# Kernel optimization log

Measured on AMD Instinct MI355X. Metric: run time of the kernel, lower is better.

The kernel has to match this reference:

```python
import jax, jax.numpy as jnp
import numpy as np

D_MODEL = 1024
N_HEAD = 16
DIM_PER_HEAD = D_MODEL // N_HEAD
B, S = 8, 1024


def setup_inputs() -> dict:
    key = jax.random.key(0)
    ks = jax.random.split(key, 12)
    s = 0.02
    return {
        "k": jax.random.normal(ks[0], (B, S, D_MODEL), jnp.float32),
        "v": jax.random.normal(ks[1], (B, S, D_MODEL), jnp.float32),
        "q": jax.random.normal(ks[2], (B, S, D_MODEL), jnp.float32),
        "attn_mask": jax.random.randint(ks[3], (B, S, S), 0, 2, jnp.int32),
        "Wk": jax.random.normal(ks[4], (D_MODEL, D_MODEL), jnp.float32) * s,
        "bk": jnp.zeros((D_MODEL,), jnp.float32),
        "Wv": jax.random.normal(ks[5], (D_MODEL, D_MODEL), jnp.float32) * s,
        "bv": jnp.zeros((D_MODEL,), jnp.float32),
        "Wq": jax.random.normal(ks[6], (D_MODEL, D_MODEL), jnp.float32) * s,
        "bq": jnp.zeros((D_MODEL,), jnp.float32),
        "Wo": jax.random.normal(ks[7], (D_MODEL, D_MODEL), jnp.float32) * s,
        "bo": jnp.zeros((D_MODEL,), jnp.float32),
    }


def reference(k, v, q, attn_mask, Wk, bk, Wv, bv, Wq, bq, Wo, bo):
    batch, key_len, _ = k.shape
    query_len = q.shape[1]
    scale = 1.0 / jnp.sqrt(jnp.float32(DIM_PER_HEAD))

    def split_heads(x):  # [b, s, d] -> [b, h, s, dh]
        return x.reshape(batch, -1, N_HEAD, DIM_PER_HEAD).transpose(0, 2, 1, 3)

    key_up = split_heads(k @ Wk + bk)
    value_up = split_heads(v @ Wv + bv)
    query_up = split_heads(q @ Wq + bq) * scale

    # [b, h, q, k] scores; mask nonzero entries with -inf (masked_fill_ semantics)
    scores = jnp.einsum("bhqd,bhkd->bhqk", query_up, key_up)
    scores = jnp.where(attn_mask[:, None, :, :] != 0, -jnp.inf, scores)
    attn = jax.nn.softmax(scores, axis=-1)
    # NOTE: original applies dropout but discards the result; attn (pre-dropout) is used.
    context = jnp.einsum("bhqk,bhkd->bhqd", attn, value_up)
    context = context.transpose(0, 2, 1, 3).reshape(batch, query_len, D_MODEL)
    output = context @ Wo + bo
    attn_mean = attn.sum(axis=1) / N_HEAD  # [b, q, k]
    return output, attn_mean
```

## Files before the change

kernel.cpp:

```cpp
#include <hip/hip_runtime.h>
#include <hip/hip_bf16.h>

typedef unsigned short u16;
typedef unsigned int u32;
typedef __attribute__((ext_vector_type(8))) short bf16x8;
typedef __attribute__((ext_vector_type(4))) float f32x4;
typedef __attribute__((ext_vector_type(4))) u16 u16x4;
typedef __attribute__((ext_vector_type(4))) u32 u32x4;

#define DEV static __device__ __forceinline__

DEV u16 f2bf(float x) {
  unsigned u = __builtin_bit_cast(unsigned, x);
  u += 0x7fffu + ((u >> 16) & 1u);
  return (u16)(u >> 16);
}
DEV float bf2f(u16 u) { return __builtin_bit_cast(float, ((unsigned)u) << 16); }

DEV u32 cvtpk(float lo, float hi) {
  u32 r;
  asm("v_cvt_pk_bf16_f32 %0, %1, %2" : "=v"(r) : "v"(lo), "v"(hi));
  return r;
}

DEV void glds16(const u16* g, u16* l) {
  __builtin_amdgcn_global_load_lds(
      (const __attribute__((address_space(1))) void*)g,
      (__attribute__((address_space(3))) void*)l, 16, 0, 0);
}

__global__ __launch_bounds__(256) void xcvt(
    const float* __restrict__ k, const float* __restrict__ v,
    const float* __restrict__ q, u16* __restrict__ Xb) {
  const size_t i0 = (size_t)blockIdx.x * 256 + threadIdx.x;
  for (size_t t = i0; t < 6291456; t += 524288) {
    const size_t e = t * 4;
    const float* src = (e < 8388608) ? k + e
                     : (e < 16777216) ? v + (e - 8388608)
                     : q + (e - 16777216);
    const f32x4 x = *(const f32x4*)src;
    u16x4 o;
#pragma unroll
    for (int r = 0; r < 4; ++r) o[r] = f2bf(x[r]);
    *(u16x4*)&Xb[e] = o;
  }
}

__global__ __launch_bounds__(256) void transpose_w(
    const float* __restrict__ w0, const float* __restrict__ w1,
    const float* __restrict__ w2, const float* __restrict__ w3,
    u16* __restrict__ out) {
  __shared__ u16 tile[32][33];
  const int mat = blockIdx.y;
  const float* in = (mat == 0) ? w0 : (mat == 1) ? w1 : (mat == 2) ? w2 : w3;
  u16* o = out + (size_t)mat * 1048576;
  const int bk = ((int)blockIdx.x & 31) << 5;
  const int bn = ((int)blockIdx.x >> 5) << 5;
  const int tx = threadIdx.x & 31, ty = threadIdx.x >> 5;
#pragma unroll
  for (int i = 0; i < 32; i += 8)
    tile[ty + i][tx] = f2bf(in[(size_t)(bk + ty + i) * 1024 + bn + tx]);
  __syncthreads();
#pragma unroll
  for (int i = 0; i < 32; i += 8)
    o[(size_t)(bn + ty + i) * 1024 + bk + tx] = tile[tx][ty + i];
}

__global__ __launch_bounds__(256) void maskpack(
    const int* __restrict__ mask, unsigned long long* __restrict__ Mb) {
  const int qt = blockIdx.x, b = blockIdx.y;
  const int tid = threadIdx.x;
  const int w = tid >> 6, l = tid & 63;
  const int ln = l & 15, lg = l >> 4;
  const int* Mp = mask + ((size_t)b << 20) + ((size_t)(qt << 4) << 10);
  unsigned long long m = 0ull;
#pragma unroll
  for (int t = 0; t < 16; ++t) {
    const int key = (w << 8) + (t << 4) + ln;
#pragma unroll
    for (int r = 0; r < 4; ++r) {
      const int row = (lg << 2) + r;
      if (Mp[((size_t)row << 10) + key] != 0) m |= 1ull << ((t << 2) + r);
    }
  }
  Mb[((((size_t)b << 6) + qt) << 8) + tid] = m;
}

__global__ __launch_bounds__(256) void gemm_qkv(
    const u16* __restrict__ Xb, const u16* __restrict__ WTall,
    const float* __restrict__ bK, const float* __restrict__ bV,
    const float* __restrict__ bQ,
    u16* __restrict__ Kup, u16* __restrict__ VupT, u16* __restrict__ Qup) {
  __shared__ u16 As[4096];
  __shared__ u16 Bs[4096];
  const int mode = blockIdx.y;
  const u16* A = Xb + (size_t)mode * 8388608;
  const u16* Bw = WTall + (size_t)mode * 1048576;
  const float* bias = (mode == 0) ? bK : (mode == 1) ? bV : bQ;

  const int tid = threadIdx.x;
  const int w = tid >> 6, l = tid & 63;
  const int ln = l & 15, lg = l >> 4, kg8 = lg << 3;
  const int wr = w >> 1, wc = w & 1;
  const int mb = ((int)blockIdx.x >> 3) << 7;
  const int nb = ((int)blockIdx.x & 7) << 7;

  const int srow = (w << 5) + (l >> 2);
  const int sseg = (l & 3) << 3;
  const u16* Ag0 = A + (size_t)(mb + srow) * 1024 + sseg;
  const u16* Bg0 = Bw + (size_t)(nb + srow) * 1024 + sseg;
  u16* Al0 = As + srow * 32 + sseg;
  u16* Bl0 = Bs + srow * 32 + sseg;

  f32x4 acc[4][4] = {};
  const int ar = (wr << 6) + ln;
  const int br = (wc << 6) + ln;

  for (int k0 = 0; k0 < 1024; k0 += 32) {
    glds16(Ag0 + k0, Al0);
    glds16(Ag0 + 16384 + k0, Al0 + 512);
    glds16(Bg0 + k0, Bl0);
    glds16(Bg0 + 16384 + k0, Bl0 + 512);
    __syncthreads();
    bf16x8 aa[4], bb[4];
#pragma unroll
    for (int mt = 0; mt < 4; ++mt) aa[mt] = *(const bf16x8*)&As[(ar + (mt << 4)) * 32 + kg8];
#pragma unroll
    for (int nt = 0; nt < 4; ++nt) bb[nt] = *(const bf16x8*)&Bs[(br + (nt << 4)) * 32 + kg8];
#pragma unroll
    for (int mt = 0; mt < 4; ++mt)
#pragma unroll
      for (int nt = 0; nt < 4; ++nt)
        acc[mt][nt] = __builtin_amdgcn_mfma_f32_16x16x32_bf16(aa[mt], bb[nt], acc[mt][nt], 0, 0, 0);
    __syncthreads();
  }

  const float scale = (mode == 2) ? 0.125f : 1.0f;
#pragma unroll
  for (int mt = 0; mt < 4; ++mt) {
    const int m0 = mb + (wr << 6) + (mt << 4) + (lg << 2);
    const int bb_ = m0 >> 10, s0 = m0 & 1023;
#pragma unroll
    for (int nt = 0; nt < 4; ++nt) {
      const int n = nb + (wc << 6) + (nt << 4) + ln;
      const float bval = bias[n];
      const int h = n >> 6, dh = n & 63;
      const size_t bh = (size_t)(bb_ * 16 + h);
      if (mode == 1) {
        const int wv = dh >> 4, lnv = dh & 15;
        const int kk = s0 >> 5, lgv = (s0 >> 3) & 3, e0 = s0 & 7;
        u16x4 pk;
#pragma unroll
        for (int r = 0; r < 4; ++r) pk[r] = f2bf(acc[mt][nt][r] + bval);
        *(u16x4*)&VupT[(bh << 16) + (wv << 14) + (kk << 9) + (lgv << 7) +
                       (lnv << 3) + e0] = pk;
      } else if (mode == 0) {
        const int half = dh >> 5, lg2 = (dh >> 3) & 3, e = dh & 7;
        const int T = s0 >> 4;
        u16* base = Kup + (bh << 16) + (T << 10) + (half << 9) + (lg2 << 7) + e;
#pragma unroll
        for (int r = 0; r < 4; ++r)
          base[((s0 & 15) + r) << 3] = f2bf(acc[mt][nt][r] + bval);
      } else {
#pragma unroll
        for (int r = 0; r < 4; ++r)
          Qup[((bh << 10) + s0 + r) * 64 + dh] =
              f2bf((acc[mt][nt][r] + bval) * scale);
      }
    }
  }
}

__global__ __launch_bounds__(256) void gemm_out(
    const u16* __restrict__ Ctx, const u16* __restrict__ WTall,
    const float* __restrict__ bO, float* __restrict__ Out) {
  __shared__ u16 As[4096];
  __shared__ u16 Bs[4096];
  const u16* Bw = WTall + 3145728;

  const int tid = threadIdx.x;
  const int w = tid >> 6, l = tid & 63;
  const int ln = l & 15, lg = l >> 4, kg8 = lg << 3;
  const int wr = w >> 1, wc = w & 1;
  const int mb = ((int)blockIdx.x >> 3) << 7;
  const int nb = ((int)blockIdx.x & 7) << 7;

  const int srow = (w << 5) + (l >> 2);
  const int sseg = (l & 3) << 3;
  const u16* Ag0 = Ctx + (size_t)(mb + srow) * 1024 + sseg;
  const u16* Bg0 = Bw + (size_t)(nb + srow) * 1024 + sseg;
  u16* Al0 = As + srow * 32 + sseg;
  u16* Bl0 = Bs + srow * 32 + sseg;

  f32x4 acc[4][4] = {};
  const int ar = (wr << 6) + ln;
  const int br = (wc << 6) + ln;

  for (int k0 = 0; k0 < 1024; k0 += 32) {
    glds16(Ag0 + k0, Al0);
    glds16(Ag0 + 16384 + k0, Al0 + 512);
    glds16(Bg0 + k0, Bl0);
    glds16(Bg0 + 16384 + k0, Bl0 + 512);
    __syncthreads();
    bf16x8 aa[4], bb[4];
#pragma unroll
    for (int mt = 0; mt < 4; ++mt) aa[mt] = *(const bf16x8*)&As[(ar + (mt << 4)) * 32 + kg8];
#pragma unroll
    for (int nt = 0; nt < 4; ++nt) bb[nt] = *(const bf16x8*)&Bs[(br + (nt << 4)) * 32 + kg8];
#pragma unroll
    for (int mt = 0; mt < 4; ++mt)
#pragma unroll
      for (int nt = 0; nt < 4; ++nt)
        acc[mt][nt] = __builtin_amdgcn_mfma_f32_16x16x32_bf16(aa[mt], bb[nt], acc[mt][nt], 0, 0, 0);
    __syncthreads();
  }
#pragma unroll
  for (int mt = 0; mt < 4; ++mt) {
    const int m0 = mb + (wr << 6) + (mt << 4) + (lg << 2);
#pragma unroll
    for (int nt = 0; nt < 4; ++nt) {
      const int n = nb + (wc << 6) + (nt << 4) + ln;
      const float bval = bO[n];
#pragma unroll
      for (int r = 0; r < 4; ++r)
        Out[(size_t)(m0 + r) * 1024 + n] = acc[mt][nt][r] + bval;
    }
  }
}

__global__ __launch_bounds__(256, 2) void attn_kernel(
    const u16* __restrict__ Qup, const u16* __restrict__ Kf,
    const u16* __restrict__ Vf, const unsigned long long* __restrict__ Mb,
    u16* __restrict__ Ctx, u16* __restrict__ Pp) {
  __shared__ u16 P_lds[16 * 1024];
  __shared__ float red_s[4][16];
  __shared__ float invs[16];

  const int tid = threadIdx.x;
  const int w = tid >> 6, l = tid & 63;
  const int ln = l & 15, lg = l >> 4;
  const int kg8 = lg << 3;

  const int bid = (int)blockIdx.x;
  const int b = bid & 7;
  const int idx = bid >> 3;
  const int qt = idx & 63;
  const int hs = idx >> 6;
  const int qb = qt << 4;

  const unsigned long long mbits = Mb[((((size_t)b << 6) + qt) << 8) + tid];

  u32x4 accp[8];

#pragma unroll 1
  for (int hh = 0; hh < 8; ++hh) {
    const int h = (hs << 3) + hh;
    const size_t bh = (size_t)(b * 16 + h);
    const u16* Qp = Qup + ((bh << 10) + qb) * 64;
    const u16* Kb = Kf + (bh << 16);
    const u16* Vb = Vf + (bh << 16) + ((size_t)w << 14);

    const bf16x8 qa0 = *(const bf16x8*)&Qp[ln * 64 + kg8];
    const bf16x8 qa1 = *(const bf16x8*)&Qp[ln * 64 + 32 + kg8];

    bf16x8 ka[3], kb[3];
#pragma unroll
    for (int p = 0; p < 3; ++p) {
      const int To = ((w << 4) + p) << 10;
      ka[p] = *(const bf16x8*)&Kb[To + (l << 3)];
      kb[p] = *(const bf16x8*)&Kb[To + 512 + (l << 3)];
    }

    float rsum[4] = {0, 0, 0, 0};
#pragma unroll
    for (int t = 0; t < 16; ++t) {
      const int s = t % 3;
      const bf16x8 k0 = ka[s], k1 = kb[s];
      if (t + 3 < 16) {
        const int To = ((w << 4) + t + 3) << 10;
        ka[s] = *(const bf16x8*)&Kb[To + (l << 3)];
        kb[s] = *(const bf16x8*)&Kb[To + 512 + (l << 3)];
      }
      f32x4 c = {0, 0, 0, 0};
      c = __builtin_amdgcn_mfma_f32_16x16x32_bf16(qa0, k0, c, 0, 0, 0);
      c = __builtin_amdgcn_mfma_f32_16x16x32_bf16(qa1, k1, c, 0, 0, 0);
      const int key = (w << 8) + (t << 4) + ln;
      float p[4];
#pragma unroll
      for (int r = 0; r < 4; ++r) {
        p[r] = ((mbits >> ((t << 2) + r)) & 1ull) ? 0.0f : __expf(c[r] - 4.0f);
        rsum[r] += p[r];
      }
      const u32 pk01 = cvtpk(p[0], p[1]);
      const u32 pk23 = cvtpk(p[2], p[3]);
      const int r0 = lg << 2;
      *(u16*)((char*)P_lds + ((((r0 + 0) << 11) + (key << 1)) ^ (((r0 + 0) & 7) << 4))) = (u16)pk01;
      *(u16*)((char*)P_lds + ((((r0 + 1) << 11) + (key << 1)) ^ (((r0 + 1) & 7) << 4))) = (u16)(pk01 >> 16);
      *(u16*)((char*)P_lds + ((((r0 + 2) << 11) + (key << 1)) ^ (((r0 + 2) & 7) << 4))) = (u16)pk23;
      *(u16*)((char*)P_lds + ((((r0 + 3) << 11) + (key << 1)) ^ (((r0 + 3) & 7) << 4))) = (u16)(pk23 >> 16);
    }
#pragma unroll
    for (int off = 1; off < 16; off <<= 1) {
#pragma unroll
      for (int r = 0; r < 4; ++r) rsum[r] += __shfl_xor(rsum[r], off);
    }
    if (ln == 0) {
#pragma unroll
      for (int r = 0; r < 4; ++r) red_s[w][(lg << 2) + r] = rsum[r];
    }

    bf16x8 vr[4];
#pragma unroll
    for (int p = 0; p < 4; ++p)
      vr[p] = *(const bf16x8*)&Vb[(p << 9) + (l << 3)];

    __syncthreads();
    float inv[4];
#pragma unroll
    for (int r = 0; r < 4; ++r) {
      const int row = (lg << 2) + r;
      inv[r] = 1.0f / (red_s[0][row] + red_s[1][row] + red_s[2][row] + red_s[3][row]);
    }
    if (ln == 0) {
#pragma unroll
      for (int r = 0; r < 4; ++r) invs[(lg << 2) + r] = inv[r];
    }

    f32x4 c0 = {0, 0, 0, 0}, c1 = {0, 0, 0, 0};
#pragma unroll
    for (int kk = 0; kk < 32; ++kk) {
      const int s = kk & 3;
      const bf16x8 vb = vr[s];
      if (kk + 4 < 32)
        vr[s] = *(const bf16x8*)&Vb[((kk + 4) << 9) + (l << 3)];
      const int a0 = ((ln << 11) + (((kk << 5) + kg8) << 1)) ^ ((ln & 7) << 4);
      const bf16x8 pa = *(const bf16x8*)((const char*)P_lds + a0);
      if (kk & 1)
        c1 = __builtin_amdgcn_mfma_f32_16x16x32_bf16(pa, vb, c1, 0, 0, 0);
      else
        c0 = __builtin_amdgcn_mfma_f32_16x16x32_bf16(pa, vb, c0, 0, 0, 0);
    }
    {
      const u32 q01 = cvtpk((c0[0] + c1[0]) * inv[0], (c0[1] + c1[1]) * inv[1]);
      const u32 q23 = cvtpk((c0[2] + c1[2]) * inv[2], (c0[3] + c1[3]) * inv[3]);
      u16* Cp = &Ctx[(((size_t)b << 10) + qb + (lg << 2)) * 1024 + (h << 6) + (w << 4) + ln];
      Cp[0] = (u16)q01;
      Cp[1024] = (u16)(q01 >> 16);
      Cp[2048] = (u16)q23;
      Cp[3072] = (u16)(q23 >> 16);
    }

    {
      const int row = tid >> 4;
      const float iv = invs[row];
#pragma unroll
      for (int i = 0; i < 8; ++i) {
        const int chunk = (tid & 15) + (i << 4);
        const int bo_ = ((row << 11) + (chunk << 4)) ^ ((row & 7) << 4);
        const u32x4 pu = *(const u32x4*)((const char*)P_lds + bo_);
        u32x4 o;
#pragma unroll
        for (int j = 0; j < 4; ++j) {
          const float plo = __builtin_bit_cast(float, pu[j] << 16) * iv;
          const float phi = __builtin_bit_cast(float, pu[j] & 0xFFFF0000u) * iv;
          if (hh == 0) {
            o[j] = cvtpk(plo, phi);
          } else {
            const u32 a = accp[i][j];
            const float alo = __builtin_bit_cast(float, a << 16);
            const float ahi = __builtin_bit_cast(float, a & 0xFFFF0000u);
            o[j] = cvtpk(alo + plo, ahi + phi);
          }
        }
        accp[i] = o;
      }
    }
    __syncthreads();
  }

  {
    const int row = tid >> 4;
    u16* Pg = Pp + ((size_t)hs << 23) + (((size_t)b << 10) + qb + row) * 1024;
#pragma unroll
    for (int i = 0; i < 8; ++i) {
      const int chunk = (tid & 15) + (i << 4);
      *(u32x4*)&Pg[chunk << 3] = accp[i];
    }
  }
}

__global__ __launch_bounds__(256) void combine2(
    const u16* __restrict__ Pp, float* __restrict__ Am) {
  const size_t i = ((size_t)blockIdx.x * 256 + threadIdx.x) * 8;
  const u16x4* q0 = (const u16x4*)&Pp[i];
  const u16x4* q1 = (const u16x4*)&Pp[8388608 + i];
  const u16x4 a0 = q0[0], a1 = q0[1], b0 = q1[0], b1 = q1[1];
  f32x4 lo, hi;
#pragma unroll
  for (int r = 0; r < 4; ++r) {
    lo[r] = (bf2f(a0[r]) + bf2f(b0[r])) * 0.0625f;
    hi[r] = (bf2f(a1[r]) + bf2f(b1[r])) * 0.0625f;
  }
  *(f32x4*)&Am[i] = lo;
  *(f32x4*)&Am[i + 4] = hi;
}

extern "C" void kernel_launch(void* const* d_in, const int* in_sizes, int n_in,
                              void* d_out, int out_size, void* d_ws, size_t ws_size,
                              hipStream_t stream) {
  const float* k_in = (const float*)d_in[0];
  const float* v_in = (const float*)d_in[1];
  const float* q_in = (const float*)d_in[2];
  const int* mask = (const int*)d_in[3];
  const float* Wk = (const float*)d_in[4];
  const float* bk = (const float*)d_in[5];
  const float* Wv = (const float*)d_in[6];
  const float* bv = (const float*)d_in[7];
  const float* Wq = (const float*)d_in[8];
  const float* bq = (const float*)d_in[9];
  const float* Wo = (const float*)d_in[10];
  const float* bo = (const float*)d_in[11];

  float* out = (float*)d_out;
  float* amean = out + (size_t)8 * 1024 * 1024;

  u16* ws = (u16*)d_ws;
  u16* WT = ws;
  u16* Xb = ws + 4194304;
  unsigned long long* Mb = (unsigned long long*)(ws + 29360128);
  u16* Pp = ws + 37748736;
  u16* Kf   = ws + 71303168;
  u16* Vf   = ws + 79691776;
  u16* Qup  = ws + 88080384;
  u16* Ctx  = ws + 96468992;

  xcvt<<<2048, 256, 0, stream>>>(k_in, v_in, q_in, Xb);
  transpose_w<<<dim3(1024, 4), dim3(256), 0, stream>>>(Wk, Wv, Wq, Wo, WT);
  maskpack<<<dim3(64, 8), dim3(256), 0, stream>>>(mask, Mb);
  gemm_qkv<<<dim3(512, 3), dim3(256), 0, stream>>>(
      Xb, WT, bk, bv, bq, Kf, Vf, Qup);
  attn_kernel<<<dim3(1024), dim3(256), 0, stream>>>(
      Qup, Kf, Vf, Mb, Ctx, Pp);
  combine2<<<4096, 256, 0, stream>>>(Pp, amean);
  gemm_out<<<512, 256, 0, stream>>>(Ctx, WT, bo, out);
}
```

Before: 309.3 us.

## Merge prep kernels, fold combine into out-GEMM, use K=64 swizzled LDS tiles

The three preprocessing kernels (input cast, weight transpose, mask packing) become one launch that dispatches on block index. The attention-mean combine kernel is folded into the output GEMM launch as extra blocks. Both GEMMs now stage 64-wide K tiles with an XOR-swizzled LDS layout, halving the number of barriers per K loop and avoiding bank conflicts on fragment reads. The cost is doubled shared memory per block and divergent block roles within one launch.

```diff
diff --git a/kernel.cpp b/kernel.cpp
--- a/kernel.cpp
+++ b/kernel.cpp
@@ -29,61 +29,64 @@
       (__attribute__((address_space(3))) void*)l, 16, 0, 0);
 }
 
-__global__ __launch_bounds__(256) void xcvt(
+__global__ __launch_bounds__(256) void prep(
     const float* __restrict__ k, const float* __restrict__ v,
-    const float* __restrict__ q, u16* __restrict__ Xb) {
-  const size_t i0 = (size_t)blockIdx.x * 256 + threadIdx.x;
-  for (size_t t = i0; t < 6291456; t += 524288) {
-    const size_t e = t * 4;
-    const float* src = (e < 8388608) ? k + e
-                     : (e < 16777216) ? v + (e - 8388608)
-                     : q + (e - 16777216);
-    const f32x4 x = *(const f32x4*)src;
-    u16x4 o;
-#pragma unroll
-    for (int r = 0; r < 4; ++r) o[r] = f2bf(x[r]);
-    *(u16x4*)&Xb[e] = o;
-  }
-}
-
-__global__ __launch_bounds__(256) void transpose_w(
+    const float* __restrict__ q,
     const float* __restrict__ w0, const float* __restrict__ w1,
     const float* __restrict__ w2, const float* __restrict__ w3,
-    u16* __restrict__ out) {
+    const int* __restrict__ mask,
+    u16* __restrict__ Xb, u16* __restrict__ WT,
+    unsigned long long* __restrict__ Mb) {
   __shared__ u16 tile[32][33];
-  const int mat = blockIdx.y;
-  const float* in = (mat == 0) ? w0 : (mat == 1) ? w1 : (mat == 2) ? w2 : w3;
-  u16* o = out + (size_t)mat * 1048576;
-  const int bk = ((int)blockIdx.x & 31) << 5;
-  const int bn = ((int)blockIdx.x >> 5) << 5;
-  const int tx = threadIdx.x & 31, ty = threadIdx.x >> 5;
-#pragma unroll
-  for (int i = 0; i < 32; i += 8)
-    tile[ty + i][tx] = f2bf(in[(size_t)(bk + ty + i) * 1024 + bn + tx]);
-  __syncthreads();
-#pragma unroll
-  for (int i = 0; i < 32; i += 8)
-    o[(size_t)(bn + ty + i) * 1024 + bk + tx] = tile[tx][ty + i];
-}
-
-__global__ __launch_bounds__(256) void maskpack(
-    const int* __restrict__ mask, unsigned long long* __restrict__ Mb) {
-  const int qt = blockIdx.x, b = blockIdx.y;
+  const int bid = (int)blockIdx.x;
   const int tid = threadIdx.x;
-  const int w = tid >> 6, l = tid & 63;
-  const int ln = l & 15, lg = l >> 4;
-  const int* Mp = mask + ((size_t)b << 20) + ((size_t)(qt << 4) << 10);
-  unsigned long long m = 0ull;
-#pragma unroll
-  for (int t = 0; t < 16; ++t) {
-    const int key = (w << 8) + (t << 4) + ln;
-#pragma unroll
-    for (int r = 0; r < 4; ++r) {
-      const int row = (lg << 2) + r;
-      if (Mp[((size_t)row << 10) + key] != 0) m |= 1ull << ((t << 2) + r);
-    }
-  }
-  Mb[((((size_t)b << 6) + qt) << 8) + tid] = m;
+  if (bid < 2048) {
+    const size_t i0 = (size_t)bid * 256 + tid;
+    for (size_t t = i0; t < 6291456; t += 524288) {
+      const size_t e = t * 4;
+      const float* src = (e < 8388608) ? k + e
+                       : (e < 16777216) ? v + (e - 8388608)
+                       : q + (e - 16777216);
+      const f32x4 x = *(const f32x4*)src;
+      u16x4 o;
+#pragma unroll
+      for (int r = 0; r < 4; ++r) o[r] = f2bf(x[r]);
+      *(u16x4*)&Xb[e] = o;
+    }
+  } else if (bid < 6144) {
+    const int lb = bid - 2048;
+    const int mat = lb >> 10;
+    const int bx = lb & 1023;
+    const float* in = (mat == 0) ? w0 : (mat == 1) ? w1 : (mat == 2) ? w2 : w3;
+    u16* o = WT + (size_t)mat * 1048576;
+    const int bk = (bx & 31) << 5;
+    const int bn = (bx >> 5) << 5;
+    const int tx = tid & 31, ty = tid >> 5;
+#pragma unroll
+    for (int i = 0; i < 32; i += 8)
+      tile[ty + i][tx] = f2bf(in[(size_t)(bk + ty + i) * 1024 + bn + tx]);
+    __syncthreads();
+#pragma unroll
+    for (int i = 0; i < 32; i += 8)
+      o[(size_t)(bn + ty + i) * 1024 + bk + tx] = tile[tx][ty + i];
+  } else {
+    const int lb = bid - 6144;
+    const int qt = lb & 63, b = lb >> 6;
+    const int w = tid >> 6, l = tid & 63;
+    const int ln = l & 15, lg = l >> 4;
+    const int* Mp = mask + ((size_t)b << 20) + ((size_t)(qt << 4) << 10);
+    unsigned long long m = 0ull;
+#pragma unroll
+    for (int t = 0; t < 16; ++t) {
+      const int key = (w << 8) + (t << 4) + ln;
+#pragma unroll
+      for (int r = 0; r < 4; ++r) {
+        const int row = (lg << 2) + r;
+        if (Mp[((size_t)row << 10) + key] != 0) m |= 1ull << ((t << 2) + r);
+      }
+    }
+    Mb[((((size_t)b << 6) + qt) << 8) + tid] = m;
+  }
 }
 
 __global__ __launch_bounds__(256) void gemm_qkv(
@@ -91,8 +94,8 @@
     const float* __restrict__ bK, const float* __restrict__ bV,
     const float* __restrict__ bQ,
     u16* __restrict__ Kup, u16* __restrict__ VupT, u16* __restrict__ Qup) {
-  __shared__ u16 As[4096];
-  __shared__ u16 Bs[4096];
+  __shared__ u16 As[8192];
+  __shared__ u16 Bs[8192];
   const int mode = blockIdx.y;
   const u16* A = Xb + (size_t)mode * 8388608;
   const u16* Bw = WTall + (size_t)mode * 1048576;
@@ -100,38 +103,42 @@
 
   const int tid = threadIdx.x;
   const int w = tid >> 6, l = tid & 63;
-  const int ln = l & 15, lg = l >> 4, kg8 = lg << 3;
+  const int ln = l & 15, lg = l >> 4;
   const int wr = w >> 1, wc = w & 1;
   const int mb = ((int)blockIdx.x >> 3) << 7;
   const int nb = ((int)blockIdx.x & 7) << 7;
 
-  const int srow = (w << 5) + (l >> 2);
-  const int sseg = (l & 3) << 3;
-  const u16* Ag0 = A + (size_t)(mb + srow) * 1024 + sseg;
-  const u16* Bg0 = Bw + (size_t)(nb + srow) * 1024 + sseg;
-  u16* Al0 = As + srow * 32 + sseg;
-  u16* Bl0 = Bs + srow * 32 + sseg;
-
   f32x4 acc[4][4] = {};
   const int ar = (wr << 6) + ln;
   const int br = (wc << 6) + ln;
-
-  for (int k0 = 0; k0 < 1024; k0 += 32) {
-    glds16(Ag0 + k0, Al0);
-    glds16(Ag0 + 16384 + k0, Al0 + 512);
-    glds16(Bg0 + k0, Bl0);
-    glds16(Bg0 + 16384 + k0, Bl0 + 512);
-    __syncthreads();
-    bf16x8 aa[4], bb[4];
-#pragma unroll
-    for (int mt = 0; mt < 4; ++mt) aa[mt] = *(const bf16x8*)&As[(ar + (mt << 4)) * 32 + kg8];
-#pragma unroll
-    for (int nt = 0; nt < 4; ++nt) bb[nt] = *(const bf16x8*)&Bs[(br + (nt << 4)) * 32 + kg8];
-#pragma unroll
-    for (int mt = 0; mt < 4; ++mt)
-#pragma unroll
-      for (int nt = 0; nt < 4; ++nt)
-        acc[mt][nt] = __builtin_amdgcn_mfma_f32_16x16x32_bf16(aa[mt], bb[nt], acc[mt][nt], 0, 0, 0);
+  const int x7 = ln & 7;
+
+  for (int k0 = 0; k0 < 1024; k0 += 64) {
+#pragma unroll
+    for (int i = 0; i < 4; ++i) {
+      const int off = (i << 11) + (tid << 3);
+      const int row = off >> 6;
+      const int sc = ((((off >> 3) & 7) ^ (row & 7)) << 3);
+      glds16(A + (size_t)(mb + row) * 1024 + k0 + sc, As + off);
+      glds16(Bw + (size_t)(nb + row) * 1024 + k0 + sc, Bs + off);
+    }
+    __syncthreads();
+#pragma unroll
+    for (int kk = 0; kk < 2; ++kk) {
+      const int g = (kk << 2) + lg;
+      const int rc = (g ^ x7) << 3;
+      bf16x8 aa[4], bb[4];
+#pragma unroll
+      for (int mt = 0; mt < 4; ++mt) {
+        aa[mt] = *(const bf16x8*)&As[(ar + (mt << 4)) * 64 + rc];
+        bb[mt] = *(const bf16x8*)&Bs[(br + (mt << 4)) * 64 + rc];
+      }
+#pragma unroll
+      for (int mt = 0; mt < 4; ++mt)
+#pragma unroll
+        for (int nt = 0; nt < 4; ++nt)
+          acc[mt][nt] = __builtin_amdgcn_mfma_f32_16x16x32_bf16(aa[mt], bb[nt], acc[mt][nt], 0, 0, 0);
+    }
     __syncthreads();
   }
 
@@ -173,45 +180,68 @@
 
 __global__ __launch_bounds__(256) void gemm_out(
     const u16* __restrict__ Ctx, const u16* __restrict__ WTall,
-    const float* __restrict__ bO, float* __restrict__ Out) {
-  __shared__ u16 As[4096];
-  __shared__ u16 Bs[4096];
+    const float* __restrict__ bO, const u16* __restrict__ Pp,
+    float* __restrict__ Out) {
+  __shared__ u16 As[8192];
+  __shared__ u16 Bs[8192];
+  const int bid = (int)blockIdx.x;
+  const int tid = threadIdx.x;
+
+  if (bid >= 512) {
+    float* Am = Out + 8388608;
+    const size_t i = ((size_t)(bid - 512) * 256 + tid) * 8;
+    const u16x4* q0 = (const u16x4*)&Pp[i];
+    const u16x4* q1 = (const u16x4*)&Pp[8388608 + i];
+    const u16x4 a0 = q0[0], a1 = q0[1], b0 = q1[0], b1 = q1[1];
+    f32x4 lo, hi;
+#pragma unroll
+    for (int r = 0; r < 4; ++r) {
+      lo[r] = (bf2f(a0[r]) + bf2f(b0[r])) * 0.0625f;
+      hi[r] = (bf2f(a1[r]) + bf2f(b1[r])) * 0.0625f;
+    }
+    *(f32x4*)&Am[i] = lo;
+    *(f32x4*)&Am[i + 4] = hi;
+    return;
+  }
+
   const u16* Bw = WTall + 3145728;
-
-  const int tid = threadIdx.x;
   const int w = tid >> 6, l = tid & 63;
-  const int ln = l & 15, lg = l >> 4, kg8 = lg << 3;
+  const int ln = l & 15, lg = l >> 4;
   const int wr = w >> 1, wc = w & 1;
-  const int mb = ((int)blockIdx.x >> 3) << 7;
-  const int nb = ((int)blockIdx.x & 7) << 7;
-
-  const int srow = (w << 5) + (l >> 2);
-  const int sseg = (l & 3) << 3;
-  const u16* Ag0 = Ctx + (size_t)(mb + srow) * 1024 + sseg;
-  const u16* Bg0 = Bw + (size_t)(nb + srow) * 1024 + sseg;
-  u16* Al0 = As + srow * 32 + sseg;
-  u16* Bl0 = Bs + srow * 32 + sseg;
+  const int mb = (bid >> 3) << 7;
+  const int nb = (bid & 7) << 7;
 
   f32x4 acc[4][4] = {};
   const int ar = (wr << 6) + ln;
   const int br = (wc << 6) + ln;
-
-  for (int k0 = 0; k0 < 1024; k0 += 32) {
-    glds16(Ag0 + k0, Al0);
-    glds16(Ag0 + 16384 + k0, Al0 + 512);
-    glds16(Bg0 + k0, Bl0);
-    glds16(Bg0 + 16384 + k0, Bl0 + 512);
-    __syncthreads();
-    bf16x8 aa[4], bb[4];
-#pragma unroll
-    for (int mt = 0; mt < 4; ++mt) aa[mt] = *(const bf16x8*)&As[(ar + (mt << 4)) * 32 + kg8];
-#pragma unroll
-    for (int nt = 0; nt < 4; ++nt) bb[nt] = *(const bf16x8*)&Bs[(br + (nt << 4)) * 32 + kg8];
-#pragma unroll
-    for (int mt = 0; mt < 4; ++mt)
-#pragma unroll
-      for (int nt = 0; nt < 4; ++nt)
-        acc[mt][nt] = __builtin_amdgcn_mfma_f32_16x16x32_bf16(aa[mt], bb[nt], acc[mt][nt], 0, 0, 0);
+  const int x7 = ln & 7;
+
+  for (int k0 = 0; k0 < 1024; k0 += 64) {
+#pragma unroll
+    for (int i = 0; i < 4; ++i) {
+      const int off = (i << 11) + (tid << 3);
+      const int row = off >> 6;
+      const int sc = ((((off >> 3) & 7) ^ (row & 7)) << 3);
+      glds16(Ctx + (size_t)(mb + row) * 1024 + k0 + sc, As + off);
+      glds16(Bw + (size_t)(nb + row) * 1024 + k0 + sc, Bs + off);
+    }
+    __syncthreads();
+#pragma unroll
+    for (int kk = 0; kk < 2; ++kk) {
+      const int g = (kk << 2) + lg;
+      const int rc = (g ^ x7) << 3;
+      bf16x8 aa[4], bb[4];
+#pragma unroll
+      for (int mt = 0; mt < 4; ++mt) {
+        aa[mt] = *(const bf16x8*)&As[(ar + (mt << 4)) * 64 + rc];
+        bb[mt] = *(const bf16x8*)&Bs[(br + (mt << 4)) * 64 + rc];
+      }
+#pragma unroll
+      for (int mt = 0; mt < 4; ++mt)
+#pragma unroll
+        for (int nt = 0; nt < 4; ++nt)
+          acc[mt][nt] = __builtin_amdgcn_mfma_f32_16x16x32_bf16(aa[mt], bb[nt], acc[mt][nt], 0, 0, 0);
+    }
     __syncthreads();
   }
 #pragma unroll
@@ -387,22 +417,6 @@
       *(u32x4*)&Pg[chunk << 3] = accp[i];
     }
   }
-}
-
-__global__ __launch_bounds__(256) void combine2(
-    const u16* __restrict__ Pp, float* __restrict__ Am) {
-  const size_t i = ((size_t)blockIdx.x * 256 + threadIdx.x) * 8;
-  const u16x4* q0 = (const u16x4*)&Pp[i];
-  const u16x4* q1 = (const u16x4*)&Pp[8388608 + i];
-  const u16x4 a0 = q0[0], a1 = q0[1], b0 = q1[0], b1 = q1[1];
-  f32x4 lo, hi;
-#pragma unroll
-  for (int r = 0; r < 4; ++r) {
-    lo[r] = (bf2f(a0[r]) + bf2f(b0[r])) * 0.0625f;
-    hi[r] = (bf2f(a1[r]) + bf2f(b1[r])) * 0.0625f;
-  }
-  *(f32x4*)&Am[i] = lo;
-  *(f32x4*)&Am[i + 4] = hi;
 }
 
 extern "C" void kernel_launch(void* const* d_in, const int* in_sizes, int n_in,
@@ -422,7 +436,6 @@
   const float* bo = (const float*)d_in[11];
 
   float* out = (float*)d_out;
-  float* amean = out + (size_t)8 * 1024 * 1024;
 
   u16* ws = (u16*)d_ws;
   u16* WT = ws;
@@ -434,13 +447,11 @@
   u16* Qup  = ws + 88080384;
   u16* Ctx  = ws + 96468992;
 
-  xcvt<<<2048, 256, 0, stream>>>(k_in, v_in, q_in, Xb);
-  transpose_w<<<dim3(1024, 4), dim3(256), 0, stream>>>(Wk, Wv, Wq, Wo, WT);
-  maskpack<<<dim3(64, 8), dim3(256), 0, stream>>>(mask, Mb);
+  prep<<<6656, 256, 0, stream>>>(k_in, v_in, q_in, Wk, Wv, Wq, Wo, mask,
+                                 Xb, WT, Mb);
   gemm_qkv<<<dim3(512, 3), dim3(256), 0, stream>>>(
       Xb, WT, bk, bv, bq, Kf, Vf, Qup);
   attn_kernel<<<dim3(1024), dim3(256), 0, stream>>>(
       Qup, Kf, Vf, Mb, Ctx, Pp);
-  combine2<<<4096, 256, 0, stream>>>(Pp, amean);
-  gemm_out<<<512, 256, 0, stream>>>(Ctx, WT, bo, out);
-}
+  gemm_out<<<4608, 256, 0, stream>>>(Ctx, WT, bo, Pp, out);
+}
```

Measured after the change: 297.9 us. -3.7%, faster.
